# Optimization experiments

Hardware: AMD Instinct MI355X
Metric: run time of the kernel (lower is better)

## Reference

```python
import jax, jax.numpy as jnp
import numpy as np
from jax import lax

N_FREE = 10
DT = 0.1
COMP = 4


def setup_inputs() -> dict:
    key = jax.random.key(0)
    kx, kw = jax.random.split(key)
    B, D = 256, 16384
    nodes = D // COMP  # 4096
    x = jax.random.normal(kx, (B, D), dtype=jnp.float32)
    # Hopfield-style node-coupling matrix (learned parameter), small init for stable relaxation
    W = jax.random.normal(kw, (nodes, nodes), dtype=jnp.float32) * 0.02
    return {"x": x, "W": W}


def reference(x, W):
    B, D = x.shape
    nodes = D // COMP
    # project scalar features to multivectors (B, nodes, comp)
    x_mv = x.reshape(B, nodes, COMP)
    W_sym = 0.5 * (W + W.T)  # symmetric coupling => well-defined energy

    def step(h, _):
        rho = jnp.tanh(h)                                      # (B, nodes, comp)
        drive = jnp.einsum('nm,bmc->bnc', W_sym, rho) + x_mv   # recurrent + input coupling
        grad_E = h - (1.0 - rho * rho) * drive                 # dE/dh
        return h - DT * grad_E, None

    h_free, _ = lax.scan(step, x_mv, None, length=N_FREE)
    return h_free[..., 0]  # scalar (grade-0) component, (B, nodes)
```

## Files before the change

kernel.cpp:

```cpp
#include <hip/hip_runtime.h>
#include <hip/hip_bf16.h>


#define BATCH   256
#define NODES   4096
#define MDIM    1024
#define KDIM    4096
#define DLEN    16384

typedef __attribute__((ext_vector_type(8))) __bf16 bf16x8;
typedef __attribute__((ext_vector_type(4))) float  f32x4;

static __device__ __forceinline__ unsigned short f32_to_bf16(float f) {
    unsigned int u = __float_as_uint(f);
    u += 0x7fffu + ((u >> 16) & 1u);
    return (unsigned short)(u >> 16);
}

__global__ __launch_bounds__(256)
void symw_kernel(const float* __restrict__ W, unsigned short* __restrict__ Wb) {
    __shared__ float Ta[64][64];
    __shared__ float Tb[64][65];
    const int tn = blockIdx.y, tm = blockIdx.x;
    const int c  = threadIdx.x & 63;
    const int r0 = threadIdx.x >> 6;
#pragma unroll
    for (int rr = 0; rr < 16; ++rr) {
        int r = r0 * 16 + rr;
        Ta[r][c] = W[(size_t)(tn * 64 + r) * 4096 + tm * 64 + c];
        Tb[r][c] = W[(size_t)(tm * 64 + r) * 4096 + tn * 64 + c];
    }
    __syncthreads();
#pragma unroll
    for (int rr = 0; rr < 16; ++rr) {
        int r = r0 * 16 + rr;
        float v = 0.5f * (Ta[r][c] + Tb[c][r]);
        Wb[(size_t)(tn * 64 + r) * 4096 + tm * 64 + c] = f32_to_bf16(v);
    }
}

__global__ __launch_bounds__(256)
void init_kernel(const float* __restrict__ x, float* __restrict__ h,
                 unsigned short* __restrict__ R0) {
    int idx = blockIdx.x * blockDim.x + threadIdx.x;
    int b = idx >> 12;
    int m = idx & 4095;
    f32x4 xv = *(const f32x4*)(x + (size_t)idx * 4);
    *(f32x4*)(h + (size_t)idx * 4) = xv;
#pragma unroll
    for (int c = 0; c < 4; ++c) {
        R0[((size_t)(b * 4 + c)) * (size_t)KDIM + m] = f32_to_bf16(tanhf(xv[c]));
    }
}

#define BM 64
#define BN 128
#define BK 64

__global__ __launch_bounds__(256, 2)
void step_kernel(const unsigned short* __restrict__ Rcur,
                 const unsigned short* __restrict__ Wb,
                 const float* __restrict__ x,
                 float* __restrict__ h,
                 unsigned short* __restrict__ Rnxt,
                 float* __restrict__ out) {
    __shared__ unsigned short As[2][BM * BK];
    __shared__ unsigned short Bs[2][BN * BK];

    const int tid  = threadIdx.x;
    const int bx   = blockIdx.x;
    const int by   = blockIdx.y;
    const int rowA0 = by * BM;
    const int rowB0 = bx * BN;

    const int w    = tid >> 6;
    const int lane = tid & 63;
    const int m0   = (w >> 1) * 32;
    const int n0   = (w & 1) * 64;
    const int lr   = lane & 15;
    const int lk   = lane >> 4;

    const int chA0 = tid,        chA1 = tid + 256;

    f32x4 acc[2][4];
#pragma unroll
    for (int mi = 0; mi < 2; ++mi)
#pragma unroll
        for (int ni = 0; ni < 4; ++ni)
            acc[mi][ni] = (f32x4){0.f, 0.f, 0.f, 0.f};

#define STAGE(buf, k0)                                                          \
    do {                                                                        \
        _Pragma("unroll")                                                       \
        for (int j = 0; j < 2; ++j) {                                           \
            int chunk = tid + 256 * j;                                          \
            int row = chunk >> 3, cs = chunk & 7;                               \
            int cg = cs ^ (row & 7);                                            \
            const unsigned short* g =                                           \
                Rcur + (size_t)(rowA0 + row) * KDIM + (k0) + cg * 8;            \
            __builtin_amdgcn_global_load_lds(                                   \
                (const __attribute__((address_space(1))) void*)g,               \
                (__attribute__((address_space(3))) void*)(As[buf] + chunk * 8), \
                16, 0, 0);                                                      \
        }                                                                       \
        _Pragma("unroll")                                                       \
        for (int j = 0; j < 4; ++j) {                                           \
            int chunk = tid + 256 * j;                                          \
            int row = chunk >> 3, cs = chunk & 7;                               \
            int cg = cs ^ (row & 7);                                            \
            const unsigned short* g =                                           \
                Wb + (size_t)(rowB0 + row) * KDIM + (k0) + cg * 8;              \
            __builtin_amdgcn_global_load_lds(                                   \
                (const __attribute__((address_space(1))) void*)g,               \
                (__attribute__((address_space(3))) void*)(Bs[buf] + chunk * 8), \
                16, 0, 0);                                                      \
        }                                                                       \
    } while (0)

    STAGE(0, 0);
    asm volatile("s_waitcnt vmcnt(0)" ::: "memory");
    __builtin_amdgcn_s_barrier();

    const int NT = KDIM / BK;
    for (int t = 0; t < NT; ++t) {
        const int cur = t & 1;
        if (t + 1 < NT) STAGE(cur ^ 1, (t + 1) * BK);

        const unsigned short* Ab = As[cur];
        const unsigned short* Bb = Bs[cur];
#pragma unroll
        for (int kk = 0; kk < 2; ++kk) {
            bf16x8 a[2], b[4];
#pragma unroll
            for (int mi = 0; mi < 2; ++mi) {
                int row = m0 + mi * 16 + lr;
                int slot = (kk * 4 + lk) ^ (row & 7);
                a[mi] = *(const bf16x8*)(Ab + row * BK + slot * 8);
            }
#pragma unroll
            for (int ni = 0; ni < 4; ++ni) {
                int row = n0 + ni * 16 + lr;
                int slot = (kk * 4 + lk) ^ (row & 7);
                b[ni] = *(const bf16x8*)(Bb + row * BK + slot * 8);
            }
#pragma unroll
            for (int mi = 0; mi < 2; ++mi)
#pragma unroll
                for (int ni = 0; ni < 4; ++ni)
                    acc[mi][ni] = __builtin_amdgcn_mfma_f32_16x16x32_bf16(
                        a[mi], b[ni], acc[mi][ni], 0, 0, 0);
        }
        asm volatile("s_waitcnt vmcnt(0)" ::: "memory");
        __builtin_amdgcn_s_barrier();
    }
#undef STAGE

#pragma unroll
    for (int mi = 0; mi < 2; ++mi) {
        int i0 = rowA0 + m0 + mi * 16 + lk * 4;
        int b  = i0 >> 2;
#pragma unroll
        for (int ni = 0; ni < 4; ++ni) {
            int n = rowB0 + n0 + ni * 16 + lr;
            size_t hidx = (size_t)b * DLEN + (size_t)n * 4;
            f32x4 h4 = *(const f32x4*)(h + hidx);
            f32x4 x4 = *(const f32x4*)(x + hidx);
            f32x4 hn;
#pragma unroll
            for (int r = 0; r < 4; ++r) {
                float hv   = h4[r];
                float rho  = tanhf(hv);
                float drive = acc[mi][ni][r] + x4[r];
                float hnew = 0.9f * hv + 0.1f * (1.0f - rho * rho) * drive;
                hn[r] = hnew;
                Rnxt[(size_t)(i0 + r) * KDIM + n] = f32_to_bf16(tanhf(hnew));
            }
            *(f32x4*)(h + hidx) = hn;
            if (out) out[(size_t)b * NODES + n] = hn[0];
        }
    }
}

extern "C" void kernel_launch(void* const* d_in, const int* in_sizes, int n_in,
                              void* d_out, int out_size, void* d_ws, size_t ws_size,
                              hipStream_t stream) {
    const float* x = (const float*)d_in[0];
    const float* W = (const float*)d_in[1];
    float* out = (float*)d_out;

    char* ws = (char*)d_ws;
    unsigned short* Wb = (unsigned short*)(ws);
    unsigned short* R0 = (unsigned short*)(ws + ((size_t)32 << 20));
    unsigned short* R1 = (unsigned short*)(ws + ((size_t)40 << 20));
    float*          h  = (float*)(ws + ((size_t)48 << 20));

    symw_kernel<<<dim3(64, 64), 256, 0, stream>>>(W, Wb);
    init_kernel<<<dim3(4096), 256, 0, stream>>>(x, h, R0);

    unsigned short* rc = R0;
    unsigned short* rn = R1;
    for (int s = 0; s < 10; ++s) {
        step_kernel<<<dim3(32, 16), 256, 0, stream>>>(
            rc, Wb, x, h, rn, (s == 9) ? out : nullptr);
        unsigned short* t = rc; rc = rn; rn = t;
    }
}
```

Baseline: 667.8 us.

## Triple-buffer LDS tiles with partial vmcnt waits in step GEMM

Moves the step kernel's GEMM main loop from double to triple buffering in LDS. Tiles are prefetched two iterations ahead, and each iteration waits with a partial s_waitcnt vmcnt(6) so only the oldest stage must have landed, keeping one stage of global loads in flight during compute. Per-thread global and LDS load offsets are also precomputed once instead of recomputed inside each stage. LDS use rises from 48KB to 72KB per block, which may limit co-residency under launch_bounds(256,2). Because the buffer indices are runtime variables, the compiler may fall back to dynamic LDS addressing.

```diff
diff --git a/kernel.cpp b/kernel.cpp
--- a/kernel.cpp
+++ b/kernel.cpp
@@ -56,6 +56,7 @@
 #define BM 64
 #define BN 128
 #define BK 64
+#define NT (KDIM / BK)
 
 __global__ __launch_bounds__(256, 2)
 void step_kernel(const unsigned short* __restrict__ Rcur,
@@ -64,8 +65,8 @@
                  float* __restrict__ h,
                  unsigned short* __restrict__ Rnxt,
                  float* __restrict__ out) {
-    __shared__ unsigned short As[2][BM * BK];
-    __shared__ unsigned short Bs[2][BN * BK];
+    __shared__ unsigned short As[3][BM * BK];
+    __shared__ unsigned short Bs[3][BN * BK];
 
     const int tid  = threadIdx.x;
     const int bx   = blockIdx.x;
@@ -80,7 +81,24 @@
     const int lr   = lane & 15;
     const int lk   = lane >> 4;
 
-    const int chA0 = tid,        chA1 = tid + 256;
+    size_t offA[2], offB[4];
+    int ldsoA[2], ldsoB[4];
+#pragma unroll
+    for (int j = 0; j < 2; ++j) {
+        int chunk = tid + 256 * j;
+        int row = chunk >> 3, cs = chunk & 7;
+        int cg = cs ^ (row & 7);
+        offA[j]  = (size_t)(rowA0 + row) * KDIM + cg * 8;
+        ldsoA[j] = chunk * 8;
+    }
+#pragma unroll
+    for (int j = 0; j < 4; ++j) {
+        int chunk = tid + 256 * j;
+        int row = chunk >> 3, cs = chunk & 7;
+        int cg = cs ^ (row & 7);
+        offB[j]  = (size_t)(rowB0 + row) * KDIM + cg * 8;
+        ldsoB[j] = chunk * 8;
+    }
 
     f32x4 acc[2][4];
 #pragma unroll
@@ -93,67 +111,63 @@
     do {                                                                        \
         _Pragma("unroll")                                                       \
         for (int j = 0; j < 2; ++j) {                                           \
-            int chunk = tid + 256 * j;                                          \
-            int row = chunk >> 3, cs = chunk & 7;                               \
-            int cg = cs ^ (row & 7);                                            \
-            const unsigned short* g =                                           \
-                Rcur + (size_t)(rowA0 + row) * KDIM + (k0) + cg * 8;            \
             __builtin_amdgcn_global_load_lds(                                   \
-                (const __attribute__((address_space(1))) void*)g,               \
-                (__attribute__((address_space(3))) void*)(As[buf] + chunk * 8), \
+                (const __attribute__((address_space(1))) void*)(Rcur + offA[j] + (k0)), \
+                (__attribute__((address_space(3))) void*)(As[buf] + ldsoA[j]),  \
                 16, 0, 0);                                                      \
         }                                                                       \
         _Pragma("unroll")                                                       \
         for (int j = 0; j < 4; ++j) {                                           \
-            int chunk = tid + 256 * j;                                          \
-            int row = chunk >> 3, cs = chunk & 7;                               \
-            int cg = cs ^ (row & 7);                                            \
-            const unsigned short* g =                                           \
-                Wb + (size_t)(rowB0 + row) * KDIM + (k0) + cg * 8;              \
             __builtin_amdgcn_global_load_lds(                                   \
-                (const __attribute__((address_space(1))) void*)g,               \
-                (__attribute__((address_space(3))) void*)(Bs[buf] + chunk * 8), \
+                (const __attribute__((address_space(1))) void*)(Wb + offB[j] + (k0)), \
+                (__attribute__((address_space(3))) void*)(Bs[buf] + ldsoB[j]),  \
                 16, 0, 0);                                                      \
         }                                                                       \
     } while (0)
 
+#define COMPUTE(buf)                                                            \
+    do {                                                                        \
+        _Pragma("unroll")                                                       \
+        for (int kk = 0; kk < 2; ++kk) {                                        \
+            bf16x8 a[2], b[4];                                                  \
+            _Pragma("unroll")                                                   \
+            for (int mi = 0; mi < 2; ++mi) {                                    \
+                int row = m0 + mi * 16 + lr;                                    \
+                int slot = (kk * 4 + lk) ^ (row & 7);                           \
+                a[mi] = *(const bf16x8*)(As[buf] + row * BK + slot * 8);        \
+            }                                                                   \
+            _Pragma("unroll")                                                   \
+            for (int ni = 0; ni < 4; ++ni) {                                    \
+                int row = n0 + ni * 16 + lr;                                    \
+                int slot = (kk * 4 + lk) ^ (row & 7);                           \
+                b[ni] = *(const bf16x8*)(Bs[buf] + row * BK + slot * 8);        \
+            }                                                                   \
+            _Pragma("unroll")                                                   \
+            for (int mi = 0; mi < 2; ++mi)                                      \
+                _Pragma("unroll")                                               \
+                for (int ni = 0; ni < 4; ++ni)                                  \
+                    acc[mi][ni] = __builtin_amdgcn_mfma_f32_16x16x32_bf16(      \
+                        a[mi], b[ni], acc[mi][ni], 0, 0, 0);                    \
+        }                                                                       \
+    } while (0)
+
     STAGE(0, 0);
-    asm volatile("s_waitcnt vmcnt(0)" ::: "memory");
-    __builtin_amdgcn_s_barrier();
-
-    const int NT = KDIM / BK;
+    STAGE(1, BK);
+
+    int cur = 0, nxt = 1, far = 2;
     for (int t = 0; t < NT; ++t) {
-        const int cur = t & 1;
-        if (t + 1 < NT) STAGE(cur ^ 1, (t + 1) * BK);
-
-        const unsigned short* Ab = As[cur];
-        const unsigned short* Bb = Bs[cur];
-#pragma unroll
-        for (int kk = 0; kk < 2; ++kk) {
-            bf16x8 a[2], b[4];
-#pragma unroll
-            for (int mi = 0; mi < 2; ++mi) {
-                int row = m0 + mi * 16 + lr;
-                int slot = (kk * 4 + lk) ^ (row & 7);
-                a[mi] = *(const bf16x8*)(Ab + row * BK + slot * 8);
-            }
-#pragma unroll
-            for (int ni = 0; ni < 4; ++ni) {
-                int row = n0 + ni * 16 + lr;
-                int slot = (kk * 4 + lk) ^ (row & 7);
-                b[ni] = *(const bf16x8*)(Bb + row * BK + slot * 8);
-            }
-#pragma unroll
-            for (int mi = 0; mi < 2; ++mi)
-#pragma unroll
-                for (int ni = 0; ni < 4; ++ni)
-                    acc[mi][ni] = __builtin_amdgcn_mfma_f32_16x16x32_bf16(
-                        a[mi], b[ni], acc[mi][ni], 0, 0, 0);
+        if (t == NT - 1) {
+            asm volatile("s_waitcnt vmcnt(0)" ::: "memory");
+        } else {
+            asm volatile("s_waitcnt vmcnt(6)" ::: "memory");
         }
-        asm volatile("s_waitcnt vmcnt(0)" ::: "memory");
         __builtin_amdgcn_s_barrier();
+        if (t + 2 < NT) STAGE(far, (size_t)(t + 2) * BK);
+        COMPUTE(cur);
+        int tmp = cur; cur = nxt; nxt = far; far = tmp;
     }
 #undef STAGE
+#undef COMPUTE
 
 #pragma unroll
     for (int mi = 0; mi < 2; ++mi) {
```

Result: faster. 643.0 us (-3.7%).
